# Kernel tuning notes

Measured on AMD Instinct MI355X. Metric: run time of the kernel, lower is better.

The kernel has to match this reference:

```python
import jax, jax.numpy as jnp
import numpy as np

K_TOP = 8
TEMP = 1.0
GUMBEL_EPS = 1e-20
GEN_EPS = 1e-7
NEG_INF = -1e9


def _genconv(xn, src, dst, e, We, be, W1, b1, W2, b2):
    """GENConv: edge-proj, m=relu(x_src+e)+eps, per-dst softmax aggregation (t=1),
    residual add, then 2-layer MLP."""
    N = xn.shape[0]
    ep = e @ We + be                         # [E, C]
    m = jax.nn.relu(xn[src] + ep) + GEN_EPS  # [E, C]
    mx = jax.ops.segment_max(m, dst, num_segments=N)
    mx = jnp.where(jnp.isfinite(mx), mx, 0.0)
    w = jnp.exp(m - mx[dst])
    den = jax.ops.segment_sum(w, dst, num_segments=N)
    agg = jax.ops.segment_sum(w * m, dst, num_segments=N) / jnp.where(den > 0, den, 1.0)
    out = agg + xn
    return jax.nn.relu(out @ W1 + b1) @ W2 + b2


def setup_inputs() -> dict:
    key = jax.random.key(0)
    ks = jax.random.split(key, 16)
    N, E, D, ED = 1024, 16384, 128, 16
    H1, H2, OUT = 64, 64, 40
    s = 0.02
    return {
        "x": jax.random.normal(ks[0], (N, D), jnp.float32),
        "edge_attr": jax.random.normal(ks[1], (E, ED), jnp.float32),
        "gumbel_u": jax.random.uniform(ks[2], (N, N), jnp.float32),
        "mlp_w": jax.random.normal(ks[3], (ED + 2 * D, 1), jnp.float32) * s,
        "mlp_b": jnp.zeros((1,), jnp.float32),
        "c1_we": jax.random.normal(ks[4], (ED, D), jnp.float32) * s,
        "c1_be": jnp.zeros((D,), jnp.float32),
        "c1_w1": jax.random.normal(ks[5], (D, 2 * D), jnp.float32) * s,
        "c1_b1": jnp.zeros((2 * D,), jnp.float32),
        "c1_w2": jax.random.normal(ks[6], (2 * D, H1), jnp.float32) * s,
        "c1_b2": jnp.zeros((H1,), jnp.float32),
        "c2_we": jax.random.normal(ks[7], (ED, H1), jnp.float32) * s,
        "c2_be": jnp.zeros((H1,), jnp.float32),
        "c2_w1": jax.random.normal(ks[8], (H1, 2 * H1), jnp.float32) * s,
        "c2_b1": jnp.zeros((2 * H1,), jnp.float32),
        "c2_w2": jax.random.normal(ks[9], (2 * H1, H2), jnp.float32) * s,
        "c2_b2": jnp.zeros((H2,), jnp.float32),
        "fc_w": jax.random.normal(ks[10], (H2, OUT), jnp.float32) * s,
        "fc_b": jnp.zeros((OUT,), jnp.float32),
        "num_nodes": N,
        "edge_index": jax.random.randint(ks[11], (2, E), 0, N),
        "node_mask": jnp.ones((N,), jnp.int32),
    }


def reference(x, edge_attr, gumbel_u, mlp_w, mlp_b,
              c1_we, c1_be, c1_w1, c1_b1, c1_w2, c1_b2,
              c2_we, c2_be, c2_w1, c2_b1, c2_w2, c2_b2,
              fc_w, fc_b, num_nodes, edge_index, node_mask):
    N, D = x.shape
    src, dst = edge_index[0], edge_index[1]

    # dense adjacency (duplicate edges sum, only used as a zero/nonzero mask)
    adj = jnp.zeros((N, N), x.dtype).at[src, dst].add(1.0)

    # Edge-score MLP on concat([x_u, x_v*mask, edge_attr_dense]) decomposed
    # linearly (same math as scoring the dense [N,N,2D+ED] feature tensor).
    w_node, w_nb, w_e = mlp_w[:D], mlp_w[D:2 * D], mlp_w[2 * D:]
    s_edge = jnp.zeros((N, N), x.dtype).at[src, dst].set((edge_attr @ w_e)[:, 0])
    score = (x @ w_node) + (x @ w_nb).T * (adj > 0) + s_edge + mlp_b[0]
    score = jnp.where(adj == 0, NEG_INF, score)

    z = jax.nn.softmax(score, axis=-1)
    g = -jnp.log(-jnp.log(gumbel_u + GUMBEL_EPS) + GUMBEL_EPS)
    z = jax.nn.softmax((z + g) / TEMP, axis=-1)

    # top-k edge sampling; softmax output is strictly positive so valid_mask
    # (z>0) is always all-True and shapes stay static at N*k edges.
    _, topi = jax.lax.top_k(z, K_TOP)                       # [N, k]
    new_src = jnp.repeat(jnp.arange(N), K_TOP)
    new_dst = topi.reshape(-1)

    # match each new edge against old edge list (argmax of boolean equality,
    # unmatched edges fall back to index 0 exactly as torch argmax does)
    eq = (edge_index[0][None, :] == new_src[:, None]) & \
         (edge_index[1][None, :] == new_dst[:, None])       # [N*k, E]
    new_attr = edge_attr[jnp.argmax(eq, axis=-1)]

    h = _genconv(x, new_src, new_dst, new_attr, c1_we, c1_be, c1_w1, c1_b1, c1_w2, c1_b2)
    h = jax.nn.relu(h)
    h = _genconv(h, new_src, new_dst, new_attr, c2_we, c2_be, c2_w1, c2_b1, c2_w2, c2_b2)
    h = jax.nn.relu(h)
    out = h @ fc_w + fc_b
    # node_mask is all ones, so x[node_mask != 0] == identity; masked write
    # keeps static shapes under jit.
    return jnp.where((node_mask != 0)[:, None], out, 0.0)
```

## Files before the change

kernel.cpp:

```cpp
#include <hip/hip_runtime.h>
#include <cfloat>

#define NN   1024
#define NE   16384
#define D0   128
#define EDIM 16
#define NH1  64
#define NOUT 40
#define KTOP 8
#define NEGINF (-1000000000.0f)
#define MAXDEG 64

#define OFF_CNTS  0u
#define OFF_CNTD  4096u
#define OFF_SE    8192u
#define OFF_A     73728u
#define OFF_B     77824u
#define OFF_EM    81920u
#define OFF_SLOTS 114688u
#define OFF_SLOTD 376832u
#define OFF_H     638976u

__device__ __forceinline__ void amx(float& v, int& j, float ov, int oj) {
    if (ov > v || (ov == v && oj < j)) { v = ov; j = oj; }
}

__global__ __launch_bounds__(256) void prep_kernel(
    const float* __restrict__ x, const float* __restrict__ ea,
    const float* __restrict__ mlp_w, const int* __restrict__ ei,
    float* __restrict__ se, float* __restrict__ a, float* __restrict__ b,
    int* __restrict__ cnt_src, int* __restrict__ slot_src)
{
    const int bid = blockIdx.x, t = threadIdx.x;
    if (bid < 64) {
        int e = bid * 256 + t;
        float acc = 0.f;
        #pragma unroll
        for (int k = 0; k < EDIM; k++) acc += ea[e * EDIM + k] * mlp_w[2 * D0 + k];
        se[e] = acc;
        int s = ei[e];
        int p = atomicAdd(&cnt_src[s], 1);
        if (p < MAXDEG) slot_src[s * MAXDEG + p] = e;
    } else {
        int lane = t & 63, wid = t >> 6;
        int row = (bid - 64) * 4 + wid;
        const float* xr = x + row * D0;
        float x0 = xr[lane], x1 = xr[64 + lane];
        float sa = x0 * mlp_w[lane]       + x1 * mlp_w[64 + lane];
        float sb = x0 * mlp_w[128 + lane] + x1 * mlp_w[192 + lane];
        for (int s2 = 32; s2; s2 >>= 1) { sa += __shfl_down(sa, s2); sb += __shfl_down(sb, s2); }
        if (lane == 0) { a[row] = sa; b[row] = sb; }
    }
}

__global__ __launch_bounds__(256) void row_topk_kernel(
    const float* __restrict__ se, const float* __restrict__ mlp_b,
    const float* __restrict__ a, const float* __restrict__ b,
    const float* __restrict__ u, const int* __restrict__ ei,
    const int* __restrict__ cnt_src, const int* __restrict__ slot_src,
    int* __restrict__ em, int* __restrict__ cntd, int* __restrict__ slotd)
{
    __shared__ float sv[NN];
    __shared__ int   idmx[NN];
    __shared__ int   idmn[NN];
    __shared__ float wred[4];
    __shared__ int   wredj[4];
    __shared__ int   selj[KTOP];
    const int i = blockIdx.x, t = threadIdx.x;
    const int lane = t & 63, wid = t >> 6;
    const int rowoff = i * NN;
    const float bias = mlp_b[0];
    const float ai = a[i];

    #pragma unroll
    for (int q = 0; q < 4; q++) { int j = t + q * 256; idmx[j] = -1; idmn[j] = 0x7FFFFFFF; }
    __syncthreads();
    int deg = min(cnt_src[i], MAXDEG);
    if (t < deg) {
        int e = slot_src[i * MAXDEG + t];
        int dj = ei[NE + e];
        atomicMax(&idmx[dj], e);
        atomicMin(&idmn[dj], e);
    }
    __syncthreads();

    float lmax = NEGINF;
    #pragma unroll
    for (int q = 0; q < 4; q++) {
        int j = t + q * 256;
        int id = idmx[j];
        float s = (id >= 0) ? (((ai + b[j]) + se[id]) + bias) : NEGINF;
        sv[j] = s;
        lmax = fmaxf(lmax, s);
    }
    for (int s = 32; s; s >>= 1) lmax = fmaxf(lmax, __shfl_down(lmax, s));
    if (lane == 0) wred[wid] = lmax;
    __syncthreads();
    float rowmax = fmaxf(fmaxf(wred[0], wred[1]), fmaxf(wred[2], wred[3]));
    bool noedge = (rowmax == NEGINF);
    __syncthreads();

    float lsum = 0.f;
    #pragma unroll
    for (int q = 0; q < 4; q++) {
        int j = t + q * 256;
        float evv;
        if (noedge) evv = 1.0f;
        else { float s = sv[j]; evv = (s == NEGINF) ? 0.0f : expf(s - rowmax); }
        sv[j] = evv;
        lsum += evv;
    }
    for (int s = 32; s; s >>= 1) lsum += __shfl_down(lsum, s);
    if (lane == 0) wred[wid] = lsum;
    __syncthreads();
    float rsum = wred[0] + wred[1] + wred[2] + wred[3];
    __syncthreads();

    #pragma unroll
    for (int q = 0; q < 4; q++) {
        int j = t + q * 256;
        float z = sv[j] / rsum;
        float uu = u[rowoff + j];
        float g = -logf(-logf(uu + 1e-20f) + 1e-20f);
        sv[j] = z + g;
    }
    __syncthreads();

    for (int sel = 0; sel < KTOP; sel++) {
        float bv = -FLT_MAX; int bj = NN;
        #pragma unroll
        for (int q = 0; q < 4; q++) { int j = t + q * 256; amx(bv, bj, sv[j], j); }
        for (int s = 32; s; s >>= 1) {
            float ov = __shfl_down(bv, s); int oj = __shfl_down(bj, s);
            amx(bv, bj, ov, oj);
        }
        if (lane == 0) { wred[wid] = bv; wredj[wid] = bj; }
        __syncthreads();
        if (t == 0) {
            float v = wred[0]; int j = wredj[0];
            amx(v, j, wred[1], wredj[1]);
            amx(v, j, wred[2], wredj[2]);
            amx(v, j, wred[3], wredj[3]);
            selj[sel] = j;
            int mn = idmn[j];
            em[i * KTOP + sel] = (mn == 0x7FFFFFFF) ? 0 : mn;
            sv[j] = -FLT_MAX;
        }
        __syncthreads();
    }
    if (t < KTOP) {
        int j = selj[t];
        int n = i * KTOP + t;
        int p = atomicAdd(&cntd[j], 1);
        if (p < MAXDEG) slotd[j * MAXDEG + p] = n;
    }
}

__global__ __launch_bounds__(256) void genconv1_kernel(
    const float* __restrict__ x, const float* __restrict__ ea,
    const float* __restrict__ we_g, const float* __restrict__ be,
    const float* __restrict__ w1, const float* __restrict__ b1,
    const float* __restrict__ w2, const float* __restrict__ b2,
    const int* __restrict__ cntd, const int* __restrict__ slotd,
    const int* __restrict__ em, float* __restrict__ h)
{
    __shared__ int   slots[2][MAXDEG];
    __shared__ float eatt[2][MAXDEG * EDIM];
    __shared__ float arow[2][D0];
    __shared__ float t1s[2][2 * D0];
    const int t = threadIdx.x, sub = t >> 7, d = t & 127;
    const int r = blockIdx.x * 2 + sub;
    const int cnt = min(cntd[r], MAXDEG);
    if (d < cnt) slots[sub][d] = slotd[r * MAXDEG + d];
    __syncthreads();
    if (d == 0) {
        for (int p = 1; p < cnt; p++) {
            int v = slots[sub][p]; int q = p - 1;
            while (q >= 0 && slots[sub][q] > v) { slots[sub][q + 1] = slots[sub][q]; q--; }
            slots[sub][q + 1] = v;
        }
    }
    __syncthreads();
    for (int q = d; q < cnt * EDIM; q += 128)
        eatt[sub][q] = ea[em[slots[sub][q >> 4]] * EDIM + (q & 15)];
    __syncthreads();

    float wed[EDIM];
    #pragma unroll
    for (int k = 0; k < EDIM; k++) wed[k] = we_g[k * D0 + d];
    const float bed = be[d];

    float mxv = -FLT_MAX;
    for (int idx = 0; idx < cnt; idx++) {
        int src = slots[sub][idx] >> 3;
        float ep = bed;
        #pragma unroll
        for (int k = 0; k < EDIM; k++) ep += eatt[sub][idx * EDIM + k] * wed[k];
        float m = fmaxf(x[src * D0 + d] + ep, 0.f) + 1e-7f;
        mxv = fmaxf(mxv, m);
    }
    float den = 0.f, num = 0.f;
    for (int idx = 0; idx < cnt; idx++) {
        int src = slots[sub][idx] >> 3;
        float ep = bed;
        #pragma unroll
        for (int k = 0; k < EDIM; k++) ep += eatt[sub][idx * EDIM + k] * wed[k];
        float m = fmaxf(x[src * D0 + d] + ep, 0.f) + 1e-7f;
        float w = expf(m - mxv);
        den += w; num += w * m;
    }
    float agg = cnt ? num / (den > 0.f ? den : 1.f) : 0.f;
    arow[sub][d] = agg + x[r * D0 + d];
    __syncthreads();

    float acc0 = b1[d], acc1 = b1[d + D0];
    for (int k = 0; k < D0; k++) {
        float av = arow[sub][k];
        acc0 += av * w1[k * 2 * D0 + d];
        acc1 += av * w1[k * 2 * D0 + d + D0];
    }
    t1s[sub][d] = fmaxf(acc0, 0.f);
    t1s[sub][d + D0] = fmaxf(acc1, 0.f);
    __syncthreads();
    if (d < NH1) {
        float acc = b2[d];
        for (int k = 0; k < 2 * D0; k++) acc += t1s[sub][k] * w2[k * NH1 + d];
        h[r * NH1 + d] = fmaxf(acc, 0.f);
    }
}

__global__ __launch_bounds__(256) void genconv2_kernel(
    const float* __restrict__ h, const float* __restrict__ ea,
    const float* __restrict__ we_g, const float* __restrict__ be,
    const float* __restrict__ w1, const float* __restrict__ b1,
    const float* __restrict__ w2, const float* __restrict__ b2,
    const float* __restrict__ fcw, const float* __restrict__ fcb,
    const int* __restrict__ cntd, const int* __restrict__ slotd,
    const int* __restrict__ em, const int* __restrict__ mask,
    float* __restrict__ out)
{
    __shared__ int   slots[4][MAXDEG];
    __shared__ float eatt[4][MAXDEG * EDIM];
    __shared__ float arow[4][NH1];
    __shared__ float t2s[4][2 * NH1];
    __shared__ float h2s[4][NH1];
    const int t = threadIdx.x, sub = t >> 6, d = t & 63;
    const int r = blockIdx.x * 4 + sub;
    const int cnt = min(cntd[r], MAXDEG);
    if (d < cnt) slots[sub][d] = slotd[r * MAXDEG + d];
    __syncthreads();
    if (d == 0) {
        for (int p = 1; p < cnt; p++) {
            int v = slots[sub][p]; int q = p - 1;
            while (q >= 0 && slots[sub][q] > v) { slots[sub][q + 1] = slots[sub][q]; q--; }
            slots[sub][q + 1] = v;
        }
    }
    __syncthreads();
    for (int q = d; q < cnt * EDIM; q += 64)
        eatt[sub][q] = ea[em[slots[sub][q >> 4]] * EDIM + (q & 15)];
    __syncthreads();

    float wed[EDIM];
    #pragma unroll
    for (int k = 0; k < EDIM; k++) wed[k] = we_g[k * NH1 + d];
    const float bed = be[d];

    float mxv = -FLT_MAX;
    for (int idx = 0; idx < cnt; idx++) {
        int src = slots[sub][idx] >> 3;
        float ep = bed;
        #pragma unroll
        for (int k = 0; k < EDIM; k++) ep += eatt[sub][idx * EDIM + k] * wed[k];
        float m = fmaxf(h[src * NH1 + d] + ep, 0.f) + 1e-7f;
        mxv = fmaxf(mxv, m);
    }
    float den = 0.f, num = 0.f;
    for (int idx = 0; idx < cnt; idx++) {
        int src = slots[sub][idx] >> 3;
        float ep = bed;
        #pragma unroll
        for (int k = 0; k < EDIM; k++) ep += eatt[sub][idx * EDIM + k] * wed[k];
        float m = fmaxf(h[src * NH1 + d] + ep, 0.f) + 1e-7f;
        float w = expf(m - mxv);
        den += w; num += w * m;
    }
    float agg = cnt ? num / (den > 0.f ? den : 1.f) : 0.f;
    arow[sub][d] = agg + h[r * NH1 + d];
    __syncthreads();

    {
        float acc_a = b1[d], acc_b = b1[d + NH1];
        for (int k = 0; k < NH1; k++) {
            float av = arow[sub][k];
            acc_a += av * w1[k * 2 * NH1 + d];
            acc_b += av * w1[k * 2 * NH1 + d + NH1];
        }
        t2s[sub][d] = fmaxf(acc_a, 0.f);
        t2s[sub][d + NH1] = fmaxf(acc_b, 0.f);
    }
    __syncthreads();
    {
        float acc = b2[d];
        for (int k = 0; k < 2 * NH1; k++) acc += t2s[sub][k] * w2[k * NH1 + d];
        h2s[sub][d] = fmaxf(acc, 0.f);
    }
    __syncthreads();
    if (d < NOUT) {
        float acc = fcb[d];
        for (int k = 0; k < NH1; k++) acc += h2s[sub][k] * fcw[k * NOUT + d];
        out[r * NOUT + d] = (mask[r] != 0) ? acc : 0.f;
    }
}

extern "C" void kernel_launch(void* const* d_in, const int* in_sizes, int n_in,
                              void* d_out, int out_size, void* d_ws, size_t ws_size,
                              hipStream_t stream) {
    const float* x      = (const float*)d_in[0];
    const float* ea     = (const float*)d_in[1];
    const float* u      = (const float*)d_in[2];
    const float* mlp_w  = (const float*)d_in[3];
    const float* mlp_b  = (const float*)d_in[4];
    const float* c1_we  = (const float*)d_in[5];
    const float* c1_be  = (const float*)d_in[6];
    const float* c1_w1  = (const float*)d_in[7];
    const float* c1_b1  = (const float*)d_in[8];
    const float* c1_w2  = (const float*)d_in[9];
    const float* c1_b2  = (const float*)d_in[10];
    const float* c2_we  = (const float*)d_in[11];
    const float* c2_be  = (const float*)d_in[12];
    const float* c2_w1  = (const float*)d_in[13];
    const float* c2_b1  = (const float*)d_in[14];
    const float* c2_w2  = (const float*)d_in[15];
    const float* c2_b2  = (const float*)d_in[16];
    const float* fc_w   = (const float*)d_in[17];
    const float* fc_b   = (const float*)d_in[18];
    const int*   ei     = (const int*)d_in[20];
    const int*   mask   = (const int*)d_in[21];

    char* ws = (char*)d_ws;
    int*   cnt_src = (int*)(ws + OFF_CNTS);
    int*   cntd    = (int*)(ws + OFF_CNTD);
    float* se      = (float*)(ws + OFF_SE);
    float* a       = (float*)(ws + OFF_A);
    float* b       = (float*)(ws + OFF_B);
    int*   em      = (int*)(ws + OFF_EM);
    int*   slot_s  = (int*)(ws + OFF_SLOTS);
    int*   slotd   = (int*)(ws + OFF_SLOTD);
    float* h       = (float*)(ws + OFF_H);
    float* out     = (float*)d_out;

    hipMemsetAsync(ws + OFF_CNTS, 0, 8192, stream);
    prep_kernel<<<320, 256, 0, stream>>>(x, ea, mlp_w, ei, se, a, b, cnt_src, slot_s);
    row_topk_kernel<<<NN, 256, 0, stream>>>(se, mlp_b, a, b, u, ei, cnt_src, slot_s,
                                            em, cntd, slotd);
    genconv1_kernel<<<NN / 2, 256, 0, stream>>>(x, ea, c1_we, c1_be, c1_w1, c1_b1, c1_w2, c1_b2,
                                                cntd, slotd, em, h);
    genconv2_kernel<<<NN / 4, 256, 0, stream>>>(h, ea, c2_we, c2_be, c2_w1, c2_b1, c2_w2, c2_b2,
                                                fc_w, fc_b, cntd, slotd, em, mask, out);
}
```

Before: 156.5 us.

## Map one row per wavefront and replace block barriers with wave barriers

```diff
diff --git a/kernel.cpp b/kernel.cpp
--- a/kernel.cpp
+++ b/kernel.cpp
@@ -60,99 +60,83 @@
     const int* __restrict__ cnt_src, const int* __restrict__ slot_src,
     int* __restrict__ em, int* __restrict__ cntd, int* __restrict__ slotd)
 {
-    __shared__ float sv[NN];
-    __shared__ int   idmx[NN];
-    __shared__ int   idmn[NN];
-    __shared__ float wred[4];
-    __shared__ int   wredj[4];
-    __shared__ int   selj[KTOP];
-    const int i = blockIdx.x, t = threadIdx.x;
-    const int lane = t & 63, wid = t >> 6;
+    __shared__ int idmx[4][NN];
+    __shared__ int idmn[4][NN];
+    const int t = threadIdx.x, lane = t & 63, wid = t >> 6;
+    const int i = blockIdx.x * 4 + wid;
     const int rowoff = i * NN;
     const float bias = mlp_b[0];
     const float ai = a[i];
 
-    #pragma unroll
-    for (int q = 0; q < 4; q++) { int j = t + q * 256; idmx[j] = -1; idmn[j] = 0x7FFFFFFF; }
-    __syncthreads();
+    float uv[16];
+    #pragma unroll
+    for (int c = 0; c < 16; c++) uv[c] = u[rowoff + c * 64 + lane];
+
+    #pragma unroll
+    for (int c = 0; c < 16; c++) { idmx[wid][c * 64 + lane] = -1; idmn[wid][c * 64 + lane] = 0x7FFFFFFF; }
+    __builtin_amdgcn_wave_barrier();
     int deg = min(cnt_src[i], MAXDEG);
-    if (t < deg) {
-        int e = slot_src[i * MAXDEG + t];
+    if (lane < deg) {
+        int e = slot_src[i * MAXDEG + lane];
         int dj = ei[NE + e];
-        atomicMax(&idmx[dj], e);
-        atomicMin(&idmn[dj], e);
-    }
-    __syncthreads();
-
+        atomicMax(&idmx[wid][dj], e);
+        atomicMin(&idmn[wid][dj], e);
+    }
+    __builtin_amdgcn_wave_barrier();
+
+    float sv[16];
     float lmax = NEGINF;
     #pragma unroll
-    for (int q = 0; q < 4; q++) {
-        int j = t + q * 256;
-        int id = idmx[j];
+    for (int c = 0; c < 16; c++) {
+        int j = c * 64 + lane;
+        int id = idmx[wid][j];
         float s = (id >= 0) ? (((ai + b[j]) + se[id]) + bias) : NEGINF;
-        sv[j] = s;
+        sv[c] = s;
         lmax = fmaxf(lmax, s);
     }
     for (int s = 32; s; s >>= 1) lmax = fmaxf(lmax, __shfl_down(lmax, s));
-    if (lane == 0) wred[wid] = lmax;
-    __syncthreads();
-    float rowmax = fmaxf(fmaxf(wred[0], wred[1]), fmaxf(wred[2], wred[3]));
+    float rowmax = __shfl(lmax, 0);
     bool noedge = (rowmax == NEGINF);
-    __syncthreads();
 
     float lsum = 0.f;
     #pragma unroll
-    for (int q = 0; q < 4; q++) {
-        int j = t + q * 256;
+    for (int c = 0; c < 16; c++) {
         float evv;
         if (noedge) evv = 1.0f;
-        else { float s = sv[j]; evv = (s == NEGINF) ? 0.0f : expf(s - rowmax); }
-        sv[j] = evv;
+        else { float s = sv[c]; evv = (s == NEGINF) ? 0.0f : expf(s - rowmax); }
+        sv[c] = evv;
         lsum += evv;
     }
     for (int s = 32; s; s >>= 1) lsum += __shfl_down(lsum, s);
-    if (lane == 0) wred[wid] = lsum;
-    __syncthreads();
-    float rsum = wred[0] + wred[1] + wred[2] + wred[3];
-    __syncthreads();
-
-    #pragma unroll
-    for (int q = 0; q < 4; q++) {
-        int j = t + q * 256;
-        float z = sv[j] / rsum;
-        float uu = u[rowoff + j];
-        float g = -logf(-logf(uu + 1e-20f) + 1e-20f);
-        sv[j] = z + g;
-    }
-    __syncthreads();
-
+    float rsum = __shfl(lsum, 0);
+
+    #pragma unroll
+    for (int c = 0; c < 16; c++) {
+        float g = -logf(-logf(uv[c] + 1e-20f) + 1e-20f);
+        sv[c] = sv[c] / rsum + g;
+    }
+
+    int myj = 0;
     for (int sel = 0; sel < KTOP; sel++) {
         float bv = -FLT_MAX; int bj = NN;
         #pragma unroll
-        for (int q = 0; q < 4; q++) { int j = t + q * 256; amx(bv, bj, sv[j], j); }
+        for (int c = 0; c < 16; c++) amx(bv, bj, sv[c], c * 64 + lane);
         for (int s = 32; s; s >>= 1) {
             float ov = __shfl_down(bv, s); int oj = __shfl_down(bj, s);
             amx(bv, bj, ov, oj);
         }
-        if (lane == 0) { wred[wid] = bv; wredj[wid] = bj; }
-        __syncthreads();
-        if (t == 0) {
-            float v = wred[0]; int j = wredj[0];
-            amx(v, j, wred[1], wredj[1]);
-            amx(v, j, wred[2], wredj[2]);
-            amx(v, j, wred[3], wredj[3]);
-            selj[sel] = j;
-            int mn = idmn[j];
-            em[i * KTOP + sel] = (mn == 0x7FFFFFFF) ? 0 : mn;
-            sv[j] = -FLT_MAX;
-        }
-        __syncthreads();
-    }
-    if (t < KTOP) {
-        int j = selj[t];
-        int n = i * KTOP + t;
-        int p = atomicAdd(&cntd[j], 1);
-        if (p < MAXDEG) slotd[j * MAXDEG + p] = n;
+        int bjw = __shfl(bj, 0);
+        if (lane == sel) myj = bjw;
+        int rel = bjw - lane;
+        #pragma unroll
+        for (int c = 0; c < 16; c++) if (rel == c * 64) sv[c] = -FLT_MAX;
+    }
+    __builtin_amdgcn_wave_barrier();
+    if (lane < KTOP) {
+        int mn = idmn[wid][myj];
+        em[i * KTOP + lane] = (mn == 0x7FFFFFFF) ? 0 : mn;
+        int p = atomicAdd(&cntd[myj], 1);
+        if (p < MAXDEG) slotd[myj * MAXDEG + p] = i * KTOP + lane;
     }
 }
 
@@ -164,69 +148,85 @@
     const int* __restrict__ cntd, const int* __restrict__ slotd,
     const int* __restrict__ em, float* __restrict__ h)
 {
-    __shared__ int   slots[2][MAXDEG];
-    __shared__ float eatt[2][MAXDEG * EDIM];
-    __shared__ float arow[2][D0];
-    __shared__ float t1s[2][2 * D0];
-    const int t = threadIdx.x, sub = t >> 7, d = t & 127;
-    const int r = blockIdx.x * 2 + sub;
+    __shared__ int   slots[4][MAXDEG];
+    __shared__ float eatt[4][MAXDEG * EDIM];
+    __shared__ float arow[4][D0];
+    __shared__ float t1s[4][2 * D0];
+    const int t = threadIdx.x, lane = t & 63, wid = t >> 6;
+    const int r = blockIdx.x * 4 + wid;
     const int cnt = min(cntd[r], MAXDEG);
-    if (d < cnt) slots[sub][d] = slotd[r * MAXDEG + d];
-    __syncthreads();
-    if (d == 0) {
+    if (lane < cnt) slots[wid][lane] = slotd[r * MAXDEG + lane];
+    __builtin_amdgcn_wave_barrier();
+    if (lane == 0) {
         for (int p = 1; p < cnt; p++) {
-            int v = slots[sub][p]; int q = p - 1;
-            while (q >= 0 && slots[sub][q] > v) { slots[sub][q + 1] = slots[sub][q]; q--; }
-            slots[sub][q + 1] = v;
-        }
-    }
-    __syncthreads();
-    for (int q = d; q < cnt * EDIM; q += 128)
-        eatt[sub][q] = ea[em[slots[sub][q >> 4]] * EDIM + (q & 15)];
-    __syncthreads();
-
-    float wed[EDIM];
-    #pragma unroll
-    for (int k = 0; k < EDIM; k++) wed[k] = we_g[k * D0 + d];
-    const float bed = be[d];
-
-    float mxv = -FLT_MAX;
+            int v = slots[wid][p]; int q = p - 1;
+            while (q >= 0 && slots[wid][q] > v) { slots[wid][q + 1] = slots[wid][q]; q--; }
+            slots[wid][q + 1] = v;
+        }
+    }
+    __builtin_amdgcn_wave_barrier();
+    for (int q = lane; q < cnt * EDIM; q += 64)
+        eatt[wid][q] = ea[em[slots[wid][q >> 4]] * EDIM + (q & 15)];
+    __builtin_amdgcn_wave_barrier();
+
+    const int dA = lane, dB = lane + 64;
+    float wedA[EDIM], wedB[EDIM];
+    #pragma unroll
+    for (int k = 0; k < EDIM; k++) { wedA[k] = we_g[k * D0 + dA]; wedB[k] = we_g[k * D0 + dB]; }
+    const float bedA = be[dA], bedB = be[dB];
+
+    float mxA = -FLT_MAX, mxB = -FLT_MAX;
     for (int idx = 0; idx < cnt; idx++) {
-        int src = slots[sub][idx] >> 3;
-        float ep = bed;
-        #pragma unroll
-        for (int k = 0; k < EDIM; k++) ep += eatt[sub][idx * EDIM + k] * wed[k];
-        float m = fmaxf(x[src * D0 + d] + ep, 0.f) + 1e-7f;
-        mxv = fmaxf(mxv, m);
-    }
-    float den = 0.f, num = 0.f;
+        int src = slots[wid][idx] >> 3;
+        float epA = bedA, epB = bedB;
+        #pragma unroll
+        for (int k = 0; k < EDIM; k++) {
+            float ev = eatt[wid][idx * EDIM + k];
+            epA += ev * wedA[k];
+            epB += ev * wedB[k];
+        }
+        float mA = fmaxf(x[src * D0 + dA] + epA, 0.f) + 1e-7f;
+        float mB = fmaxf(x[src * D0 + dB] + epB, 0.f) + 1e-7f;
+        mxA = fmaxf(mxA, mA);
+        mxB = fmaxf(mxB, mB);
+    }
+    float denA = 0.f, numA = 0.f, denB = 0.f, numB = 0.f;
     for (int idx = 0; idx < cnt; idx++) {
-        int src = slots[sub][idx] >> 3;
-        float ep = bed;
-        #pragma unroll
-        for (int k = 0; k < EDIM; k++) ep += eatt[sub][idx * EDIM + k] * wed[k];
-        float m = fmaxf(x[src * D0 + d] + ep, 0.f) + 1e-7f;
-        float w = expf(m - mxv);
-        den += w; num += w * m;
-    }
-    float agg = cnt ? num / (den > 0.f ? den : 1.f) : 0.f;
-    arow[sub][d] = agg + x[r * D0 + d];
-    __syncthreads();
-
-    float acc0 = b1[d], acc1 = b1[d + D0];
+        int src = slots[wid][idx] >> 3;
+        float epA = bedA, epB = bedB;
+        #pragma unroll
+        for (int k = 0; k < EDIM; k++) {
+            float ev = eatt[wid][idx * EDIM + k];
+            epA += ev * wedA[k];
+            epB += ev * wedB[k];
+        }
+        float mA = fmaxf(x[src * D0 + dA] + epA, 0.f) + 1e-7f;
+        float mB = fmaxf(x[src * D0 + dB] + epB, 0.f) + 1e-7f;
+        float wA = expf(mA - mxA), wB = expf(mB - mxB);
+        denA += wA; numA += wA * mA;
+        denB += wB; numB += wB * mB;
+    }
+    float aggA = cnt ? numA / (denA > 0.f ? denA : 1.f) : 0.f;
+    float aggB = cnt ? numB / (denB > 0.f ? denB : 1.f) : 0.f;
+    arow[wid][dA] = aggA + x[r * D0 + dA];
+    arow[wid][dB] = aggB + x[r * D0 + dB];
+    __builtin_amdgcn_wave_barrier();
+
+    float acc[4];
+    #pragma unroll
+    for (int c = 0; c < 4; c++) acc[c] = b1[lane + 64 * c];
     for (int k = 0; k < D0; k++) {
-        float av = arow[sub][k];
-        acc0 += av * w1[k * 2 * D0 + d];
-        acc1 += av * w1[k * 2 * D0 + d + D0];
-    }
-    t1s[sub][d] = fmaxf(acc0, 0.f);
-    t1s[sub][d + D0] = fmaxf(acc1, 0.f);
-    __syncthreads();
-    if (d < NH1) {
-        float acc = b2[d];
-        for (int k = 0; k < 2 * D0; k++) acc += t1s[sub][k] * w2[k * NH1 + d];
-        h[r * NH1 + d] = fmaxf(acc, 0.f);
-    }
+        float av = arow[wid][k];
+        #pragma unroll
+        for (int c = 0; c < 4; c++) acc[c] += av * w1[k * 2 * D0 + lane + 64 * c];
+    }
+    #pragma unroll
+    for (int c = 0; c < 4; c++) t1s[wid][lane + 64 * c] = fmaxf(acc[c], 0.f);
+    __builtin_amdgcn_wave_barrier();
+
+    float acc2 = b2[lane];
+    for (int k = 0; k < 2 * D0; k++) acc2 += t1s[wid][k] * w2[k * NH1 + lane];
+    h[r * NH1 + lane] = fmaxf(acc2, 0.f);
 }
 
 __global__ __launch_bounds__(256) void genconv2_kernel(
@@ -244,22 +244,22 @@
     __shared__ float arow[4][NH1];
     __shared__ float t2s[4][2 * NH1];
     __shared__ float h2s[4][NH1];
-    const int t = threadIdx.x, sub = t >> 6, d = t & 63;
-    const int r = blockIdx.x * 4 + sub;
+    const int t = threadIdx.x, d = t & 63, wid = t >> 6;
+    const int r = blockIdx.x * 4 + wid;
     const int cnt = min(cntd[r], MAXDEG);
-    if (d < cnt) slots[sub][d] = slotd[r * MAXDEG + d];
-    __syncthreads();
+    if (d < cnt) slots[wid][d] = slotd[r * MAXDEG + d];
+    __builtin_amdgcn_wave_barrier();
     if (d == 0) {
         for (int p = 1; p < cnt; p++) {
-            int v = slots[sub][p]; int q = p - 1;
-            while (q >= 0 && slots[sub][q] > v) { slots[sub][q + 1] = slots[sub][q]; q--; }
-            slots[sub][q + 1] = v;
-        }
-    }
-    __syncthreads();
+            int v = slots[wid][p]; int q = p - 1;
+            while (q >= 0 && slots[wid][q] > v) { slots[wid][q + 1] = slots[wid][q]; q--; }
+            slots[wid][q + 1] = v;
+        }
+    }
+    __builtin_amdgcn_wave_barrier();
     for (int q = d; q < cnt * EDIM; q += 64)
-        eatt[sub][q] = ea[em[slots[sub][q >> 4]] * EDIM + (q & 15)];
-    __syncthreads();
+        eatt[wid][q] = ea[em[slots[wid][q >> 4]] * EDIM + (q & 15)];
+    __builtin_amdgcn_wave_barrier();
 
     float wed[EDIM];
     #pragma unroll
@@ -268,47 +268,47 @@
 
     float mxv = -FLT_MAX;
     for (int idx = 0; idx < cnt; idx++) {
-        int src = slots[sub][idx] >> 3;
+        int src = slots[wid][idx] >> 3;
         float ep = bed;
         #pragma unroll
-        for (int k = 0; k < EDIM; k++) ep += eatt[sub][idx * EDIM + k] * wed[k];
+        for (int k = 0; k < EDIM; k++) ep += eatt[wid][idx * EDIM + k] * wed[k];
         float m = fmaxf(h[src * NH1 + d] + ep, 0.f) + 1e-7f;
         mxv = fmaxf(mxv, m);
     }
     float den = 0.f, num = 0.f;
     for (int idx = 0; idx < cnt; idx++) {
-        int src = slots[sub][idx] >> 3;
+        int src = slots[wid][idx] >> 3;
         float ep = bed;
         #pragma unroll
-        for (int k = 0; k < EDIM; k++) ep += eatt[sub][idx * EDIM + k] * wed[k];
+        for (int k = 0; k < EDIM; k++) ep += eatt[wid][idx * EDIM + k] * wed[k];
         float m = fmaxf(h[src * NH1 + d] + ep, 0.f) + 1e-7f;
         float w = expf(m - mxv);
         den += w; num += w * m;
     }
     float agg = cnt ? num / (den > 0.f ? den : 1.f) : 0.f;
-    arow[sub][d] = agg + h[r * NH1 + d];
-    __syncthreads();
+    arow[wid][d] = agg + h[r * NH1 + d];
+    __builtin_amdgcn_wave_barrier();
 
     {
         float acc_a = b1[d], acc_b = b1[d + NH1];
         for (int k = 0; k < NH1; k++) {
-            float av = arow[sub][k];
+            float av = arow[wid][k];
             acc_a += av * w1[k * 2 * NH1 + d];
             acc_b += av * w1[k * 2 * NH1 + d + NH1];
         }
-        t2s[sub][d] = fmaxf(acc_a, 0.f);
-        t2s[sub][d + NH1] = fmaxf(acc_b, 0.f);
-    }
-    __syncthreads();
+        t2s[wid][d] = fmaxf(acc_a, 0.f);
+        t2s[wid][d + NH1] = fmaxf(acc_b, 0.f);
+    }
+    __builtin_amdgcn_wave_barrier();
     {
         float acc = b2[d];
-        for (int k = 0; k < 2 * NH1; k++) acc += t2s[sub][k] * w2[k * NH1 + d];
-        h2s[sub][d] = fmaxf(acc, 0.f);
-    }
-    __syncthreads();
+        for (int k = 0; k < 2 * NH1; k++) acc += t2s[wid][k] * w2[k * NH1 + d];
+        h2s[wid][d] = fmaxf(acc, 0.f);
+    }
+    __builtin_amdgcn_wave_barrier();
     if (d < NOUT) {
         float acc = fcb[d];
-        for (int k = 0; k < NH1; k++) acc += h2s[sub][k] * fcw[k * NOUT + d];
+        for (int k = 0; k < NH1; k++) acc += h2s[wid][k] * fcw[k * NOUT + d];
         out[r * NOUT + d] = (mask[r] != 0) ? acc : 0.f;
     }
 }
@@ -352,9 +352,9 @@
 
     hipMemsetAsync(ws + OFF_CNTS, 0, 8192, stream);
     prep_kernel<<<320, 256, 0, stream>>>(x, ea, mlp_w, ei, se, a, b, cnt_src, slot_s);
-    row_topk_kernel<<<NN, 256, 0, stream>>>(se, mlp_b, a, b, u, ei, cnt_src, slot_s,
-                                            em, cntd, slotd);
-    genconv1_kernel<<<NN / 2, 256, 0, stream>>>(x, ea, c1_we, c1_be, c1_w1, c1_b1, c1_w2, c1_b2,
+    row_topk_kernel<<<NN / 4, 256, 0, stream>>>(se, mlp_b, a, b, u, ei, cnt_src, slot_s,
+                                                em, cntd, slotd);
+    genconv1_kernel<<<NN / 4, 256, 0, stream>>>(x, ea, c1_we, c1_be, c1_w1, c1_b1, c1_w2, c1_b2,
                                                 cntd, slotd, em, h);
     genconv2_kernel<<<NN / 4, 256, 0, stream>>>(h, ea, c2_we, c2_be, c2_w1, c2_b1, c2_w2, c2_b2,
                                                 fc_w, fc_b, cntd, slotd, em, mask, out);
```

New measurement: 172.6 us. +10.3%, slower.

## Do per-wave top-k in registers, then merge candidates in one wave

Applied to the files above, without the earlier changes.

```diff
diff --git a/kernel.cpp b/kernel.cpp
--- a/kernel.cpp
+++ b/kernel.cpp
@@ -60,12 +60,11 @@
     const int* __restrict__ cnt_src, const int* __restrict__ slot_src,
     int* __restrict__ em, int* __restrict__ cntd, int* __restrict__ slotd)
 {
-    __shared__ float sv[NN];
     __shared__ int   idmx[NN];
     __shared__ int   idmn[NN];
     __shared__ float wred[4];
-    __shared__ int   wredj[4];
-    __shared__ int   selj[KTOP];
+    __shared__ float cand_v[4 * KTOP];
+    __shared__ int   cand_j[4 * KTOP];
     const int i = blockIdx.x, t = threadIdx.x;
     const int lane = t & 63, wid = t >> 6;
     const int rowoff = i * NN;
@@ -84,13 +83,14 @@
     }
     __syncthreads();
 
+    float rv[4];
     float lmax = NEGINF;
     #pragma unroll
     for (int q = 0; q < 4; q++) {
         int j = t + q * 256;
         int id = idmx[j];
         float s = (id >= 0) ? (((ai + b[j]) + se[id]) + bias) : NEGINF;
-        sv[j] = s;
+        rv[q] = s;
         lmax = fmaxf(lmax, s);
     }
     for (int s = 32; s; s >>= 1) lmax = fmaxf(lmax, __shfl_down(lmax, s));
@@ -103,56 +103,63 @@
     float lsum = 0.f;
     #pragma unroll
     for (int q = 0; q < 4; q++) {
-        int j = t + q * 256;
         float evv;
         if (noedge) evv = 1.0f;
-        else { float s = sv[j]; evv = (s == NEGINF) ? 0.0f : expf(s - rowmax); }
-        sv[j] = evv;
+        else { float s = rv[q]; evv = (s == NEGINF) ? 0.0f : expf(s - rowmax); }
+        rv[q] = evv;
         lsum += evv;
     }
     for (int s = 32; s; s >>= 1) lsum += __shfl_down(lsum, s);
     if (lane == 0) wred[wid] = lsum;
     __syncthreads();
     float rsum = wred[0] + wred[1] + wred[2] + wred[3];
-    __syncthreads();
 
     #pragma unroll
     for (int q = 0; q < 4; q++) {
         int j = t + q * 256;
-        float z = sv[j] / rsum;
+        float z = rv[q] / rsum;
         float uu = u[rowoff + j];
         float g = -logf(-logf(uu + 1e-20f) + 1e-20f);
-        sv[j] = z + g;
-    }
-    __syncthreads();
-
+        rv[q] = z + g;
+    }
+
+    float cv = -FLT_MAX; int cj = NN;
     for (int sel = 0; sel < KTOP; sel++) {
         float bv = -FLT_MAX; int bj = NN;
         #pragma unroll
-        for (int q = 0; q < 4; q++) { int j = t + q * 256; amx(bv, bj, sv[j], j); }
+        for (int q = 0; q < 4; q++) amx(bv, bj, rv[q], t + q * 256);
         for (int s = 32; s; s >>= 1) {
             float ov = __shfl_down(bv, s); int oj = __shfl_down(bj, s);
             amx(bv, bj, ov, oj);
         }
-        if (lane == 0) { wred[wid] = bv; wredj[wid] = bj; }
-        __syncthreads();
-        if (t == 0) {
-            float v = wred[0]; int j = wredj[0];
-            amx(v, j, wred[1], wredj[1]);
-            amx(v, j, wred[2], wredj[2]);
-            amx(v, j, wred[3], wredj[3]);
-            selj[sel] = j;
-            int mn = idmn[j];
-            em[i * KTOP + sel] = (mn == 0x7FFFFFFF) ? 0 : mn;
-            sv[j] = -FLT_MAX;
-        }
-        __syncthreads();
-    }
-    if (t < KTOP) {
-        int j = selj[t];
-        int n = i * KTOP + t;
-        int p = atomicAdd(&cntd[j], 1);
-        if (p < MAXDEG) slotd[j * MAXDEG + p] = n;
+        float bvw = __shfl(bv, 0); int bjw = __shfl(bj, 0);
+        if (lane == sel) { cv = bvw; cj = bjw; }
+        #pragma unroll
+        for (int q = 0; q < 4; q++) if (t + q * 256 == bjw) rv[q] = -FLT_MAX;
+    }
+    if (lane < KTOP) { cand_v[wid * KTOP + lane] = cv; cand_j[wid * KTOP + lane] = cj; }
+    __syncthreads();
+
+    if (wid == 0) {
+        float mv = (lane < 4 * KTOP) ? cand_v[lane] : -FLT_MAX;
+        int   mj = (lane < 4 * KTOP) ? cand_j[lane] : NN;
+        int myj = 0;
+        for (int sel = 0; sel < KTOP; sel++) {
+            float bv = mv; int bj = mj;
+            for (int s = 32; s; s >>= 1) {
+                float ov = __shfl_down(bv, s); int oj = __shfl_down(bj, s);
+                amx(bv, bj, ov, oj);
+            }
+            int bjw = __shfl(bj, 0);
+            if (lane == sel) myj = bjw;
+            if (mj == bjw) mv = -FLT_MAX;
+        }
+        if (lane < KTOP) {
+            int mn = idmn[myj];
+            em[i * KTOP + lane] = (mn == 0x7FFFFFFF) ? 0 : mn;
+            int p = atomicAdd(&cntd[myj], 1);
+            if (p < MAXDEG) slotd[myj * MAXDEG + p] = i * KTOP + lane;
+        }
     }
 }
 
```

Measured after the change: 158.2 us, median of 2. Within noise of the previous version (+1.1%).
